# Kernel optimization log

Hardware: AMD Instinct MI355X
Metric: run time of the kernel (lower is better)

The kernel has to match this reference:

```python
import jax, jax.numpy as jnp
import numpy as np

B, N = 2, 1024
QDIM, HEADS, DHEAD, HID, CDIM = 512, 4, 64, 64, 16
INNER = HEADS * DHEAD
LN_EPS = 1e-5


def _gelu(t):
    return jax.nn.gelu(t, approximate=False)


def setup_inputs() -> dict:
    key = jax.random.key(0)
    ks = jax.random.split(key, 32)
    inp = {
        'x': jax.random.normal(ks[0], (B, N, QDIM), jnp.float32),
        'pair_mask': jax.random.randint(ks[1], (B, N, N), 0, 2) > 0,
        'valid_mask': jax.random.randint(ks[2], (B, N), 0, 2) > 0,
        'continuous_features': jax.random.normal(ks[3], (B, N, N, CDIM), jnp.float32),
        'distance_bucket': jax.random.randint(ks[4], (B, N, N), 0, 32),
        'direction_bucket': jax.random.randint(ks[5], (B, N, N), 0, 8),
        'role_pair_id': jax.random.randint(ks[6], (B, N, N), 0, 16),
        'hop_delta': jax.random.randint(ks[7], (B, N, N), 0, 16),
        'edge_type': jax.random.randint(ks[8], (B, N, N), 0, 8),
        'shortest_path_bucket': jax.random.randint(ks[9], (B, N, N), 0, 16),
        'same_cell_type': jax.random.randint(ks[10], (B, N, N), 0, 3),
        'degree_ids': jax.random.randint(ks[11], (B, N), 0, 66),
        'cell_type_ids': jax.random.randint(ks[12], (B, N), 0, 21),
    }
    s = 0.02
    # attention projections (stored as [in, out]; y = x @ W)
    inp['Wq'] = jax.random.normal(ks[13], (QDIM, INNER), jnp.float32) * s
    inp['Wk'] = jax.random.normal(ks[14], (QDIM, INNER), jnp.float32) * s
    inp['Wv'] = jax.random.normal(ks[15], (QDIM, INNER), jnp.float32) * s
    inp['Wo'] = jax.random.normal(ks[16], (INNER, QDIM), jnp.float32) * s
    inp['bo'] = jnp.zeros((QDIM,), jnp.float32)
    # continuous MLP
    inp['mlp_w1'] = jax.random.normal(ks[17], (CDIM, HID), jnp.float32) * s
    inp['mlp_b1'] = jnp.zeros((HID,), jnp.float32)
    inp['mlp_w2'] = jax.random.normal(ks[18], (HID, HID), jnp.float32) * s
    inp['mlp_b2'] = jnp.zeros((HID,), jnp.float32)
    # embedding tables
    inp['dist_emb'] = jax.random.normal(ks[19], (32, HID), jnp.float32) * s
    inp['dir_emb'] = jax.random.normal(ks[20], (8, HID), jnp.float32) * s
    inp['role_emb'] = jax.random.normal(ks[21], (16, HID), jnp.float32) * s
    inp['hop_emb'] = jax.random.normal(ks[22], (16, HID), jnp.float32) * s
    inp['edge_emb'] = jax.random.normal(ks[23], (8, HID), jnp.float32) * s
    inp['sp_emb'] = jax.random.normal(ks[24], (16, HID), jnp.float32) * s
    deg = jax.random.normal(ks[25], (66, HID), jnp.float32) * s
    inp['deg_emb'] = deg.at[0].set(0.0)  # padding_idx=0
    ct = jax.random.normal(ks[26], (21, HID), jnp.float32) * s
    inp['ct_emb'] = ct.at[0].set(0.0)    # padding_idx=0
    inp['same_emb'] = jax.random.normal(ks[27], (3, HID), jnp.float32) * s
    # output head: LayerNorm + Linear(HID -> HEADS)
    inp['ln_g'] = jnp.ones((HID,), jnp.float32)
    inp['ln_b'] = jnp.zeros((HID,), jnp.float32)
    inp['out_w'] = jax.random.normal(ks[28], (HID, HEADS), jnp.float32) * s
    inp['out_b'] = jnp.zeros((HEADS,), jnp.float32)
    return inp


def reference(x, pair_mask, valid_mask, continuous_features, distance_bucket,
              direction_bucket, role_pair_id, hop_delta, edge_type,
              shortest_path_bucket, same_cell_type, degree_ids, cell_type_ids,
              Wq, Wk, Wv, Wo, bo, mlp_w1, mlp_b1, mlp_w2, mlp_b2,
              dist_emb, dir_emb, role_emb, hop_emb, edge_emb, sp_emb,
              deg_emb, ct_emb, same_emb, ln_g, ln_b, out_w, out_b):
    b, n, _ = x.shape
    # --- PairwiseStructuralBias ---
    pair = _gelu(continuous_features @ mlp_w1 + mlp_b1) @ mlp_w2 + mlp_b2  # [b,n,n,HID]
    pair = pair + dist_emb[distance_bucket] + dir_emb[direction_bucket] \
               + role_emb[role_pair_id] + hop_emb[hop_delta] \
               + edge_emb[edge_type] + sp_emb[shortest_path_bucket] \
               + same_emb[same_cell_type]
    deg = deg_emb[degree_ids]          # [b,n,HID]
    pair = pair + deg[:, :, None, :] + deg[:, None, :, :]
    ct = ct_emb[cell_type_ids]         # [b,n,HID]
    pair = pair + ct[:, :, None, :] + ct[:, None, :, :]
    mu = pair.mean(-1, keepdims=True)
    var = ((pair - mu) ** 2).mean(-1, keepdims=True)
    ln = (pair - mu) * jax.lax.rsqrt(var + LN_EPS) * ln_g + ln_b
    bias = _gelu(ln) @ out_w + out_b                        # [b,n,n,H]
    bias = bias * pair_mask[..., None].astype(bias.dtype)
    bias = jnp.transpose(bias, (0, 3, 1, 2))                # [b,H,i,j]
    # --- attention ---
    def split_heads(t):
        return jnp.transpose(t.reshape(b, n, HEADS, DHEAD), (0, 2, 1, 3))
    q = split_heads(x @ Wq)
    k = split_heads(x @ Wk)
    v = split_heads(x @ Wv)
    scale = DHEAD ** -0.5
    logits = jnp.einsum('bhid,bhjd->bhij', q, k) * scale + bias
    eye = jnp.eye(n, dtype=bool)
    safe_pair_mask = pair_mask | ((~valid_mask)[:, :, None] & eye[None])
    neg = -jnp.finfo(logits.dtype).max
    logits = jnp.where(safe_pair_mask[:, None], logits, neg)
    attn = jax.nn.softmax(logits, axis=-1)
    attn = attn * pair_mask[:, None].astype(attn.dtype)
    attn = attn / jnp.clip(attn.sum(-1, keepdims=True), 1e-6)
    out = jnp.einsum('bhij,bhjd->bhid', attn, v)
    out = jnp.transpose(out, (0, 2, 1, 3)).reshape(b, n, INNER)
    out = out @ Wo + bo
    return out, attn, bias
```

## Files before the change

kernel.cpp:

```cpp
#include <hip/hip_runtime.h>
#include <float.h>
#include <math.h>


#define WS_PM    0u
#define WS_VM    2097152u
#define WS_W1TB  2100224u
#define WS_W2TB  2104320u
#define WS_OWBT  2112512u
#define WS_Q     4194304u
#define WS_KT    6291456u
#define WS_V     8388608u
#define WS_AO    10485760u

typedef __attribute__((ext_vector_type(8))) short short8;
typedef __attribute__((ext_vector_type(4))) float f32x4;

__device__ __forceinline__ unsigned short f2bf(float x) {
    unsigned u = __float_as_uint(x);
    u += 0x7fffu + ((u >> 16) & 1u);
    return (unsigned short)(u >> 16);
}
__device__ __forceinline__ unsigned cvt_pk_bf16(float lo, float hi) {
    unsigned r;
    asm("v_cvt_pk_bf16_f32 %0, %1, %2" : "=v"(r) : "v"(lo), "v"(hi));
    return r;
}
__device__ __forceinline__ float gelu_fast(float x) {
    float x2 = x * x;
    float u = x * fmaf(0.0713548135f, x2, 1.5957691216f);
    float e = __expf(-u);
    return x * __builtin_amdgcn_rcpf(1.0f + e);
}
__device__ __forceinline__ float4 fma4(float s, float4 a, float4 c) {
    c.x = fmaf(s, a.x, c.x); c.y = fmaf(s, a.y, c.y);
    c.z = fmaf(s, a.z, c.z); c.w = fmaf(s, a.w, c.w);
    return c;
}
__device__ __forceinline__ float wave_max(float v) {
#pragma unroll
    for (int m = 1; m < 64; m <<= 1) v = fmaxf(v, __shfl_xor(v, m));
    return v;
}
__device__ __forceinline__ float wave_sum(float v) {
#pragma unroll
    for (int m = 1; m < 64; m <<= 1) v += __shfl_xor(v, m);
    return v;
}
__device__ __forceinline__ float4 ldg4(const float* p, int boff) {
    return *(const float4*)((const char*)p + boff);
}
__device__ __forceinline__ float4 add4(float4 a, float4 b) {
    a.x += b.x; a.y += b.y; a.z += b.z; a.w += b.w;
    return a;
}

__global__ void prep_kernel(const float* __restrict__ w1, const float* __restrict__ w2,
                            const float* __restrict__ ow,
                            unsigned short* __restrict__ w1tb,
                            unsigned short* __restrict__ w2tb,
                            unsigned short* __restrict__ owbt) {
    int t = threadIdx.x;
    for (int i = t; i < 2048; i += 256) {
        int e = i >> 5, c = i & 31;
        float v = (c < 16) ? w1[c * 64 + e] : 0.f;
        w1tb[i] = f2bf(v);
    }
    for (int i = t; i < 4096; i += 256) {
        int d = i >> 6, e = i & 63;
        w2tb[i] = f2bf(w2[e * 64 + d]);
    }
    for (int i = t; i < 1024; i += 256) {
        int h = i >> 6, e = i & 63;
        owbt[i] = (h < 4) ? f2bf(ow[e * 4 + h]) : (unsigned short)0;
    }
}

__global__ __launch_bounds__(256) void mask_kernel(const void* __restrict__ pm_raw,
                                                   const void* __restrict__ vm_raw,
                                                   unsigned char* __restrict__ pm8,
                                                   unsigned char* __restrict__ vm8) {
    __shared__ int sflag;
    int t = threadIdx.x;
    if (t == 0) sflag = 0;
    __syncthreads();
    const unsigned* p32 = (const unsigned*)pm_raw;
    unsigned acc = 0;
    for (int k = t; k < 1024; k += 256) acc |= (p32[k] & ~1u);
    if (acc) sflag = 1;
    __syncthreads();
    bool u8 = (sflag != 0);
    size_t base = (size_t)blockIdx.x * 1024;
    const unsigned char* p8 = (const unsigned char*)pm_raw;
    const int* pi = (const int*)pm_raw;
    for (int k = t; k < 1024; k += 256) {
        size_t idx = base + (size_t)k;
        pm8[idx] = u8 ? (unsigned char)(p8[idx] != 0) : (unsigned char)(pi[idx] != 0);
    }
    if (blockIdx.x == 0) {
        const unsigned char* v8 = (const unsigned char*)vm_raw;
        const int* vi = (const int*)vm_raw;
        for (int k = t; k < 2048; k += 256)
            vm8[k] = u8 ? (unsigned char)(v8[k] != 0) : (unsigned char)(vi[k] != 0);
    }
}

__global__ __launch_bounds__(256) void qkv_kernel(const float* __restrict__ x,
        const float* __restrict__ Wq, const float* __restrict__ Wk, const float* __restrict__ Wv,
        float* __restrict__ q, float* __restrict__ kt, float* __restrict__ v) {
    __shared__ float As[32][68];
    __shared__ float Bs[32][68];
    int tid = threadIdx.x;
    int bx = blockIdx.x, by = blockIdx.y;
    int mat = bx >> 2;
    const float* __restrict__ W = (mat == 0) ? Wq : ((mat == 1) ? Wk : Wv);
    int col0 = (bx & 3) * 64;
    int row0 = by * 64;
    int tx = tid & 15, ty = tid >> 4;
    int lm = tid >> 3, lk = (tid & 7) * 4;
    int bn = (tid & 15) * 4, bk = tid >> 4;
    float4 acc0 = {0,0,0,0}, acc1 = acc0, acc2 = acc0, acc3 = acc0;
    for (int k0 = 0; k0 < 512; k0 += 32) {
        float4 a0 = *(const float4*)&x[(size_t)(row0 + lm) * 512 + k0 + lk];
        float4 a1 = *(const float4*)&x[(size_t)(row0 + lm + 32) * 512 + k0 + lk];
        float4 b0 = *(const float4*)&W[(size_t)(k0 + bk) * 256 + col0 + bn];
        float4 b1 = *(const float4*)&W[(size_t)(k0 + bk + 16) * 256 + col0 + bn];
        __syncthreads();
        As[lk + 0][lm] = a0.x; As[lk + 1][lm] = a0.y; As[lk + 2][lm] = a0.z; As[lk + 3][lm] = a0.w;
        As[lk + 0][lm + 32] = a1.x; As[lk + 1][lm + 32] = a1.y; As[lk + 2][lm + 32] = a1.z; As[lk + 3][lm + 32] = a1.w;
        *(float4*)&Bs[bk][bn] = b0;
        *(float4*)&Bs[bk + 16][bn] = b1;
        __syncthreads();
#pragma unroll
        for (int kk = 0; kk < 32; ++kk) {
            float4 av = *(const float4*)&As[kk][ty * 4];
            float4 bv = *(const float4*)&Bs[kk][tx * 4];
            acc0 = fma4(av.x, bv, acc0);
            acc1 = fma4(av.y, bv, acc1);
            acc2 = fma4(av.z, bv, acc2);
            acc3 = fma4(av.w, bv, acc3);
        }
    }
#pragma unroll
    for (int r = 0; r < 4; ++r) {
        float4 a = (r == 0) ? acc0 : ((r == 1) ? acc1 : ((r == 2) ? acc2 : acc3));
        int gr = row0 + ty * 4 + r;
        int b = gr >> 10, n = gr & 1023;
        float vals[4] = {a.x, a.y, a.z, a.w};
#pragma unroll
        for (int c = 0; c < 4; ++c) {
            int cc = col0 + tx * 4 + c;
            int h = cc >> 6, d = cc & 63;
            size_t bh = (size_t)(b * 4 + h);
            float val = vals[c];
            if (mat == 0)      q[(bh * 1024 + n) * 64 + d] = val;
            else if (mat == 1) kt[(bh * 64 + d) * 1024 + n] = val;
            else               v[(bh * 1024 + n) * 64 + d] = val;
        }
    }
}

__global__ __launch_bounds__(256, 4) void pair_kernel(
        const float* __restrict__ cf,
        const int* __restrict__ i_dist, const int* __restrict__ i_dir,
        const int* __restrict__ i_role, const int* __restrict__ i_hop,
        const int* __restrict__ i_edge, const int* __restrict__ i_sp,
        const int* __restrict__ i_same,
        const int* __restrict__ deg_ids, const int* __restrict__ ct_ids,
        const float* __restrict__ e_dist, const float* __restrict__ e_dir,
        const float* __restrict__ e_role, const float* __restrict__ e_hop,
        const float* __restrict__ e_edge, const float* __restrict__ e_sp,
        const float* __restrict__ e_same, const float* __restrict__ e_deg,
        const float* __restrict__ e_ct,
        const float* __restrict__ b1, const float* __restrict__ b2,
        const unsigned short* __restrict__ w1tb, const unsigned short* __restrict__ w2tb,
        const unsigned short* __restrict__ owbt,
        const float* __restrict__ lng, const float* __restrict__ lnb,
        const float* __restrict__ outb,
        const unsigned char* __restrict__ pm,
        float* __restrict__ bias_out) {
    __shared__ alignas(8) unsigned short es[64 * 68];
    __shared__ alignas(16) unsigned short h1b[64 * 64];
    __shared__ alignas(16) unsigned short cfb[64 * 32];
    __shared__ float prm[192];
    __shared__ float bias_lds[576];

    int tid = threadIdx.x;
    int wu = __builtin_amdgcn_readfirstlane(tid >> 6);
    int lane = tid & 63;
    int m = lane & 15, g = lane >> 4;
    size_t row0 = (size_t)blockIdx.x * 64;
    int b  = (int)(row0 >> 20);
    int i  = (int)((row0 >> 10) & 1023);
    int j0 = (int)(row0 & 1023);
    int r0 = (int)row0;

    for (int k = lane; k < 192; k += 64) {
        float v;
        if (k < 64) v = b1[k];
        else if (k < 128) v = lng[k - 64];
        else v = lnb[k - 128];
        prm[k] = v;
    }
    {
        int rl = wu * 16 + (lane >> 2);
        int ch = (lane & 3) * 4;
        float4 c4 = *(const float4*)&cf[((size_t)(r0 + rl)) * 16 + ch];
        ushort4 u;
        u.x = f2bf(c4.x); u.y = f2bf(c4.y); u.z = f2bf(c4.z); u.w = f2bf(c4.w);
        *(ushort4*)&cfb[rl * 32 + ch] = u;
        ushort4 z = {0, 0, 0, 0};
        *(ushort4*)&cfb[rl * 32 + 16 + ch] = z;
    }
    {
        int di = deg_ids[b * 1024 + i];
        int ci = ct_ids[b * 1024 + i];
        int c = lane & 15;
        int rsub = lane >> 4;
        int choff = c * 16;
        float4 base4 = add4(add4(ldg4(b2, choff), ldg4(e_deg + di * 64, choff)),
                            ldg4(e_ct + ci * 64, choff));
#pragma unroll
        for (int it = 0; it < 4; ++it) {
            int row = wu * 16 + it * 4 + rsub;
            int gr = r0 + row;
            int q0 = i_dist[gr], q1 = i_dir[gr], q2 = i_role[gr], q3 = i_hop[gr],
                q4 = i_edge[gr], q5 = i_sp[gr], q6 = i_same[gr];
            int q7 = deg_ids[b * 1024 + j0 + row];
            int q8 = ct_ids[b * 1024 + j0 + row];
            float4 a = base4;
            a = add4(a, ldg4(e_dist, q0 * 256 + choff));
            a = add4(a, ldg4(e_dir,  q1 * 256 + choff));
            a = add4(a, ldg4(e_role, q2 * 256 + choff));
            a = add4(a, ldg4(e_hop,  q3 * 256 + choff));
            a = add4(a, ldg4(e_edge, q4 * 256 + choff));
            a = add4(a, ldg4(e_sp,   q5 * 256 + choff));
            a = add4(a, ldg4(e_same, q6 * 256 + choff));
            a = add4(a, ldg4(e_deg,  q7 * 256 + choff));
            a = add4(a, ldg4(e_ct,   q8 * 256 + choff));
            uint2 pk;
            pk.x = cvt_pk_bf16(a.x, a.y);
            pk.y = cvt_pk_bf16(a.z, a.w);
            *(uint2*)((char*)es + row * 136 + c * 8) = pk;
        }
    }

    f32x4 acc1[4] = {{0,0,0,0},{0,0,0,0},{0,0,0,0},{0,0,0,0}};
    {
        short8 afrag = *(const short8*)&cfb[(wu * 16 + m) * 32 + g * 8];
#pragma unroll
        for (int t = 0; t < 4; ++t) {
            short8 bfrag = *(const short8*)&w1tb[(t * 16 + m) * 32 + g * 8];
            acc1[t] = __builtin_amdgcn_mfma_f32_16x16x32_bf16(afrag, bfrag, acc1[t], 0, 0, 0);
        }
    }
#pragma unroll
    for (int tp = 0; tp < 2; ++tp) {
#pragma unroll
        for (int r = 0; r < 4; ++r) {
            int rowl = wu * 16 + g * 4 + r;
            int c0 = tp * 32 + m, c1 = c0 + 16;
            float g0 = gelu_fast(acc1[tp * 2][r] + prm[c0]);
            float g1 = gelu_fast(acc1[tp * 2 + 1][r] + prm[c1]);
            unsigned pk = cvt_pk_bf16(g0, g1);
            int swz = (rowl & 7) << 4;
            *(unsigned short*)((char*)h1b + ((rowl * 128 + c0 * 2) ^ swz)) = (unsigned short)pk;
            *(unsigned short*)((char*)h1b + ((rowl * 128 + c1 * 2) ^ swz)) = (unsigned short)(pk >> 16);
        }
    }

    f32x4 acc2[4] = {{0,0,0,0},{0,0,0,0},{0,0,0,0},{0,0,0,0}};
#pragma unroll
    for (int ks = 0; ks < 2; ++ks) {
        int rowl = wu * 16 + m;
        int byte = (rowl * 128 + ks * 64 + g * 16) ^ ((m & 7) << 4);
        short8 afrag = *(const short8*)((const char*)h1b + byte);
#pragma unroll
        for (int t = 0; t < 4; ++t) {
            short8 bfrag = *(const short8*)&w2tb[(t * 16 + m) * 64 + ks * 32 + g * 8];
            acc2[t] = __builtin_amdgcn_mfma_f32_16x16x32_bf16(afrag, bfrag, acc2[t], 0, 0, 0);
        }
    }

    float pv[4][4];
    float s[4] = {0,0,0,0}, s2[4] = {0,0,0,0};
#pragma unroll
    for (int t = 0; t < 4; ++t) {
#pragma unroll
        for (int r = 0; r < 4; ++r) {
            int rowl = wu * 16 + g * 4 + r;
            float esv = __uint_as_float((unsigned)es[rowl * 68 + t * 16 + m] << 16);
            float v = acc2[t][r] + esv;
            pv[t][r] = v;
            s[r] += v; s2[r] = fmaf(v, v, s2[r]);
        }
    }
#pragma unroll
    for (int o = 1; o < 16; o <<= 1) {
#pragma unroll
        for (int r = 0; r < 4; ++r) {
            s[r]  += __shfl_xor(s[r], o);
            s2[r] += __shfl_xor(s2[r], o);
        }
    }
    float mu[4], rs[4];
#pragma unroll
    for (int r = 0; r < 4; ++r) {
        mu[r] = s[r] * 0.015625f;
        float var = fmaxf(s2[r] * 0.015625f - mu[r] * mu[r], 0.f);
        rs[r] = rsqrtf(var + 1e-5f);
    }
#pragma unroll
    for (int tp = 0; tp < 2; ++tp) {
#pragma unroll
        for (int r = 0; r < 4; ++r) {
            int rowl = wu * 16 + g * 4 + r;
            int c0 = tp * 32 + m, c1 = c0 + 16;
            float l0 = fmaf((pv[tp * 2][r] - mu[r]) * rs[r], prm[64 + c0], prm[128 + c0]);
            float l1 = fmaf((pv[tp * 2 + 1][r] - mu[r]) * rs[r], prm[64 + c1], prm[128 + c1]);
            unsigned pk = cvt_pk_bf16(gelu_fast(l0), gelu_fast(l1));
            int swz = (rowl & 7) << 4;
            *(unsigned short*)((char*)h1b + ((rowl * 128 + c0 * 2) ^ swz)) = (unsigned short)pk;
            *(unsigned short*)((char*)h1b + ((rowl * 128 + c1 * 2) ^ swz)) = (unsigned short)(pk >> 16);
        }
    }
    f32x4 accH = {0,0,0,0};
#pragma unroll
    for (int ks = 0; ks < 2; ++ks) {
        int rowl = wu * 16 + m;
        int byte = (rowl * 128 + ks * 64 + g * 16) ^ ((m & 7) << 4);
        short8 afrag = *(const short8*)((const char*)h1b + byte);
        short8 bfrag = *(const short8*)&owbt[m * 64 + ks * 32 + g * 8];
        accH = __builtin_amdgcn_mfma_f32_16x16x32_bf16(afrag, bfrag, accH, 0, 0, 0);
    }
    if (m < 4) {
        float ob = outb[m];
#pragma unroll
        for (int r = 0; r < 4; ++r) {
            int rowl = wu * 16 + g * 4 + r;
            bias_lds[rowl * 9 + m] = accH[r] + ob;
        }
    }
    __syncthreads();
    {
        float pmv = pm[r0 + lane] ? 1.f : 0.f;
        size_t ob = (size_t)(b * 4 + wu) * 1048576u + (size_t)i * 1024u + (size_t)(j0 + lane);
        bias_out[ob] = bias_lds[lane * 9 + wu] * pmv;
    }
}

__global__ __launch_bounds__(256) void attn_kernel(
        const float* __restrict__ q, const float* __restrict__ kt, const float* __restrict__ v,
        const unsigned char* __restrict__ pm, const unsigned char* __restrict__ vm,
        const float* __restrict__ bias, float* __restrict__ attn, float* __restrict__ ao) {
    __shared__ float pbuf[4][1024];
    int tid = threadIdx.x;
    int w = tid >> 6, lane = tid & 63;
    int blk = blockIdx.x;
    int it = blk & 63;
    int bh = blk >> 6;
    int b = bh >> 2, h = bh & 3;
    int i0 = __builtin_amdgcn_readfirstlane(it * 16 + w * 4);
    const float* __restrict__ qr = q + ((size_t)bh * 1024 + i0) * 64;
    const float4* __restrict__ kt4 = (const float4*)kt;
    const float4* __restrict__ v4 = (const float4*)v;
    const float4* __restrict__ bias4 = (const float4*)bias;
    float4* __restrict__ attn4 = (float4*)attn;
    float4* __restrict__ ao4 = (float4*)ao;

    float4 lg[4][4];
#pragma unroll
    for (int jt = 0; jt < 4; ++jt) {
        float4 a0 = {0,0,0,0}, a1 = a0, a2 = a0, a3 = a0;
#pragma unroll 4
        for (int d = 0; d < 64; ++d) {
            float4 kv = kt4[((size_t)bh * 64 + d) * 256 + jt * 64 + lane];
            a0 = fma4(qr[d], kv, a0);
            a1 = fma4(qr[64 + d], kv, a1);
            a2 = fma4(qr[128 + d], kv, a2);
            a3 = fma4(qr[192 + d], kv, a3);
        }
#pragma unroll
        for (int rr = 0; rr < 4; ++rr) {
            float4 acc = (rr == 0) ? a0 : ((rr == 1) ? a1 : ((rr == 2) ? a2 : a3));
            float4 bv = bias4[((size_t)bh * 1024 + i0 + rr) * 256 + jt * 64 + lane];
            float4 l;
            l.x = fmaf(acc.x, 0.125f, bv.x);
            l.y = fmaf(acc.y, 0.125f, bv.y);
            l.z = fmaf(acc.z, 0.125f, bv.z);
            l.w = fmaf(acc.w, 0.125f, bv.w);
            lg[rr][jt] = l;
        }
    }
#pragma unroll
    for (int rr = 0; rr < 4; ++rr) {
        int i = i0 + rr;
        bool vld = vm[b * 1024 + i] != 0;
        float4 ev[4];
        float pmax = -FLT_MAX;
#pragma unroll
        for (int jt = 0; jt < 4; ++jt) {
            uchar4 m4 = *(const uchar4*)&pm[((size_t)b * 1024 + i) * 1024 + jt * 256 + lane * 4];
            int jb = jt * 256 + lane * 4;
            float4 l = lg[rr][jt];
            l.x = (m4.x || (!vld && (jb + 0) == i)) ? l.x : -FLT_MAX;
            l.y = (m4.y || (!vld && (jb + 1) == i)) ? l.y : -FLT_MAX;
            l.z = (m4.z || (!vld && (jb + 2) == i)) ? l.z : -FLT_MAX;
            l.w = (m4.w || (!vld && (jb + 3) == i)) ? l.w : -FLT_MAX;
            lg[rr][jt] = l;
            pmax = fmaxf(pmax, fmaxf(fmaxf(l.x, l.y), fmaxf(l.z, l.w)));
        }
        pmax = wave_max(pmax);
        float s1sum = 0.f;
#pragma unroll
        for (int jt = 0; jt < 4; ++jt) {
            float4 l = lg[rr][jt];
            float4 e;
            e.x = __expf(l.x - pmax); e.y = __expf(l.y - pmax);
            e.z = __expf(l.z - pmax); e.w = __expf(l.w - pmax);
            ev[jt] = e;
            s1sum += (e.x + e.y) + (e.z + e.w);
        }
        s1sum = wave_sum(s1sum);
        float inv1 = 1.f / s1sum;
        float s2sum = 0.f;
#pragma unroll
        for (int jt = 0; jt < 4; ++jt) {
            uchar4 m4 = *(const uchar4*)&pm[((size_t)b * 1024 + i) * 1024 + jt * 256 + lane * 4];
            float4 e = ev[jt];
            e.x = m4.x ? e.x * inv1 : 0.f;
            e.y = m4.y ? e.y * inv1 : 0.f;
            e.z = m4.z ? e.z * inv1 : 0.f;
            e.w = m4.w ? e.w * inv1 : 0.f;
            ev[jt] = e;
            s2sum += (e.x + e.y) + (e.z + e.w);
        }
        s2sum = wave_sum(s2sum);
        float inv2 = 1.f / fmaxf(s2sum, 1e-6f);
#pragma unroll
        for (int jt = 0; jt < 4; ++jt) {
            float4 e = ev[jt];
            e.x *= inv2; e.y *= inv2; e.z *= inv2; e.w *= inv2;
            attn4[((size_t)bh * 1024 + i) * 256 + jt * 64 + lane] = e;
            *(float4*)&pbuf[w][jt * 256 + lane * 4] = e;
        }
        __syncthreads();
        int dq = lane & 15, grp = lane >> 4;
        float4 o = {0,0,0,0};
#pragma unroll 4
        for (int t = 0; t < 64; ++t) {
            int jj = grp * 4 + t * 16;
            float4 p4 = *(const float4*)&pbuf[w][jj];
            float4 v0 = v4[((size_t)bh * 1024 + jj + 0) * 16 + dq];
            float4 v1 = v4[((size_t)bh * 1024 + jj + 1) * 16 + dq];
            float4 v2 = v4[((size_t)bh * 1024 + jj + 2) * 16 + dq];
            float4 v3 = v4[((size_t)bh * 1024 + jj + 3) * 16 + dq];
            o = fma4(p4.x, v0, o); o = fma4(p4.y, v1, o);
            o = fma4(p4.z, v2, o); o = fma4(p4.w, v3, o);
        }
        o.x += __shfl_xor(o.x, 16); o.y += __shfl_xor(o.y, 16);
        o.z += __shfl_xor(o.z, 16); o.w += __shfl_xor(o.w, 16);
        o.x += __shfl_xor(o.x, 32); o.y += __shfl_xor(o.y, 32);
        o.z += __shfl_xor(o.z, 32); o.w += __shfl_xor(o.w, 32);
        if (grp == 0) ao4[((size_t)(b * 1024 + i) * 4 + h) * 16 + dq] = o;
        __syncthreads();
    }
}

__global__ __launch_bounds__(256) void outproj_kernel(
        const float* __restrict__ ao, const float* __restrict__ Wo,
        const float* __restrict__ bo, float* __restrict__ out) {
    __shared__ float As[32][68];
    __shared__ float Bs[32][68];
    int tid = threadIdx.x;
    int bx = blockIdx.x, by = blockIdx.y;
    int col0 = bx * 64, row0 = by * 64;
    int tx = tid & 15, ty = tid >> 4;
    int lm = tid >> 3, lk = (tid & 7) * 4;
    int bn = (tid & 15) * 4, bk = tid >> 4;
    float4 acc0 = {0,0,0,0}, acc1 = acc0, acc2 = acc0, acc3 = acc0;
    for (int k0 = 0; k0 < 256; k0 += 32) {
        float4 a0 = *(const float4*)&ao[(size_t)(row0 + lm) * 256 + k0 + lk];
        float4 a1 = *(const float4*)&ao[(size_t)(row0 + lm + 32) * 256 + k0 + lk];
        float4 b0 = *(const float4*)&Wo[(size_t)(k0 + bk) * 512 + col0 + bn];
        float4 b1 = *(const float4*)&Wo[(size_t)(k0 + bk + 16) * 512 + col0 + bn];
        __syncthreads();
        As[lk + 0][lm] = a0.x; As[lk + 1][lm] = a0.y; As[lk + 2][lm] = a0.z; As[lk + 3][lm] = a0.w;
        As[lk + 0][lm + 32] = a1.x; As[lk + 1][lm + 32] = a1.y; As[lk + 2][lm + 32] = a1.z; As[lk + 3][lm + 32] = a1.w;
        *(float4*)&Bs[bk][bn] = b0;
        *(float4*)&Bs[bk + 16][bn] = b1;
        __syncthreads();
#pragma unroll
        for (int kk = 0; kk < 32; ++kk) {
            float4 av = *(const float4*)&As[kk][ty * 4];
            float4 bv = *(const float4*)&Bs[kk][tx * 4];
            acc0 = fma4(av.x, bv, acc0);
            acc1 = fma4(av.y, bv, acc1);
            acc2 = fma4(av.z, bv, acc2);
            acc3 = fma4(av.w, bv, acc3);
        }
    }
#pragma unroll
    for (int r = 0; r < 4; ++r) {
        float4 a = (r == 0) ? acc0 : ((r == 1) ? acc1 : ((r == 2) ? acc2 : acc3));
        int gr = row0 + ty * 4 + r;
        float vals[4] = {a.x, a.y, a.z, a.w};
#pragma unroll
        for (int c = 0; c < 4; ++c) {
            int gc = col0 + tx * 4 + c;
            out[(size_t)gr * 512 + gc] = vals[c] + bo[gc];
        }
    }
}

extern "C" void kernel_launch(void* const* d_in, const int* in_sizes, int n_in,
                              void* d_out, int out_size, void* d_ws, size_t ws_size,
                              hipStream_t stream) {
    (void)in_sizes; (void)n_in; (void)out_size; (void)ws_size;
    const float* x    = (const float*)d_in[0];
    const void*  pmr  = d_in[1];
    const void*  vmr  = d_in[2];
    const float* cf   = (const float*)d_in[3];
    const int* dist_b = (const int*)d_in[4];
    const int* dir_b  = (const int*)d_in[5];
    const int* role_b = (const int*)d_in[6];
    const int* hop_b  = (const int*)d_in[7];
    const int* edge_b = (const int*)d_in[8];
    const int* sp_b   = (const int*)d_in[9];
    const int* same_b = (const int*)d_in[10];
    const int* deg_ids = (const int*)d_in[11];
    const int* ct_ids  = (const int*)d_in[12];
    const float* Wq = (const float*)d_in[13];
    const float* Wk = (const float*)d_in[14];
    const float* Wv = (const float*)d_in[15];
    const float* Wo = (const float*)d_in[16];
    const float* bo = (const float*)d_in[17];
    const float* w1 = (const float*)d_in[18];
    const float* b1 = (const float*)d_in[19];
    const float* w2 = (const float*)d_in[20];
    const float* b2 = (const float*)d_in[21];
    const float* e_dist = (const float*)d_in[22];
    const float* e_dir  = (const float*)d_in[23];
    const float* e_role = (const float*)d_in[24];
    const float* e_hop  = (const float*)d_in[25];
    const float* e_edge = (const float*)d_in[26];
    const float* e_sp   = (const float*)d_in[27];
    const float* e_deg  = (const float*)d_in[28];
    const float* e_ct   = (const float*)d_in[29];
    const float* e_same = (const float*)d_in[30];
    const float* lng  = (const float*)d_in[31];
    const float* lnb  = (const float*)d_in[32];
    const float* ow   = (const float*)d_in[33];
    const float* outb = (const float*)d_in[34];

    char* ws = (char*)d_ws;
    unsigned char* pm8 = (unsigned char*)(ws + WS_PM);
    unsigned char* vm8 = (unsigned char*)(ws + WS_VM);
    unsigned short* w1tb = (unsigned short*)(ws + WS_W1TB);
    unsigned short* w2tb = (unsigned short*)(ws + WS_W2TB);
    unsigned short* owbt = (unsigned short*)(ws + WS_OWBT);
    float* q   = (float*)(ws + WS_Q);
    float* kt  = (float*)(ws + WS_KT);
    float* v   = (float*)(ws + WS_V);
    float* ao  = (float*)(ws + WS_AO);

    float* out  = (float*)d_out;
    float* attn = out + 1048576;
    float* bias = out + 9437184;

    hipLaunchKernelGGL(prep_kernel, dim3(1), dim3(256), 0, stream, w1, w2, ow, w1tb, w2tb, owbt);
    hipLaunchKernelGGL(mask_kernel, dim3(2048), dim3(256), 0, stream, pmr, vmr, pm8, vm8);
    hipLaunchKernelGGL(qkv_kernel, dim3(12, 32), dim3(256), 0, stream, x, Wq, Wk, Wv, q, kt, v);
    hipLaunchKernelGGL(pair_kernel, dim3(32768), dim3(256), 0, stream,
                       cf, dist_b, dir_b, role_b, hop_b, edge_b, sp_b, same_b, deg_ids, ct_ids,
                       e_dist, e_dir, e_role, e_hop, e_edge, e_sp, e_same, e_deg, e_ct,
                       b1, b2, w1tb, w2tb, owbt, lng, lnb, outb, pm8, bias);
    hipLaunchKernelGGL(attn_kernel, dim3(512), dim3(256), 0, stream,
                       q, kt, v, pm8, vm8, bias, attn, ao);
    hipLaunchKernelGGL(outproj_kernel, dim3(8, 32), dim3(256), 0, stream, ao, Wo, bo, out);
}
```

Before: 535.9 us.

## Transpose pair-kernel MFMAs to keep rows per lane and drop LDS staging

Swaps the MFMA operand order for the second MLP and output projections so each lane holds a full row's channels. LayerNorm statistics then need only two cross-lane shuffles, and the bias can be written straight to global memory. The continuous-feature A fragment is built in registers instead of going through LDS, and the bias staging buffer and block barrier are removed. The edge-embedding buffer gets an XOR swizzle, and launch bounds rise to 8 waves per SIMD for occupancy, which may cause register spills.

```diff
diff --git a/kernel.cpp b/kernel.cpp
--- a/kernel.cpp
+++ b/kernel.cpp
@@ -160,7 +160,7 @@
     }
 }
 
-__global__ __launch_bounds__(256, 4) void pair_kernel(
+__global__ __launch_bounds__(256, 8) void pair_kernel(
         const float* __restrict__ cf,
         const int* __restrict__ i_dist, const int* __restrict__ i_dir,
         const int* __restrict__ i_role, const int* __restrict__ i_hop,
@@ -179,11 +179,9 @@
         const float* __restrict__ outb,
         const unsigned char* __restrict__ pm,
         float* __restrict__ bias_out) {
-    __shared__ alignas(8) unsigned short es[64 * 68];
+    __shared__ alignas(16) unsigned short es[64 * 64];
     __shared__ alignas(16) unsigned short h1b[64 * 64];
-    __shared__ alignas(16) unsigned short cfb[64 * 32];
-    __shared__ float prm[192];
-    __shared__ float bias_lds[576];
+    __shared__ alignas(16) float prm[192];
 
     int tid = threadIdx.x;
     int wu = __builtin_amdgcn_readfirstlane(tid >> 6);
@@ -194,6 +192,7 @@
     int i  = (int)((row0 >> 10) & 1023);
     int j0 = (int)(row0 & 1023);
     int r0 = (int)row0;
+    int rowl = wu * 16 + m;
 
     for (int k = lane; k < 192; k += 64) {
         float v;
@@ -202,27 +201,31 @@
         else v = lnb[k - 128];
         prm[k] = v;
     }
+
+    short8 afrag1;
     {
-        int rl = wu * 16 + (lane >> 2);
-        int ch = (lane & 3) * 4;
-        float4 c4 = *(const float4*)&cf[((size_t)(r0 + rl)) * 16 + ch];
-        ushort4 u;
-        u.x = f2bf(c4.x); u.y = f2bf(c4.y); u.z = f2bf(c4.z); u.w = f2bf(c4.w);
-        *(ushort4*)&cfb[rl * 32 + ch] = u;
-        ushort4 z = {0, 0, 0, 0};
-        *(ushort4*)&cfb[rl * 32 + 16 + ch] = z;
-    }
+        if (g < 2) {
+            const float4* cp = (const float4*)&cf[((size_t)(r0 + rowl)) * 16 + g * 8];
+            float4 c0 = cp[0], c1 = cp[1];
+            unsigned p0 = cvt_pk_bf16(c0.x, c0.y), p1 = cvt_pk_bf16(c0.z, c0.w);
+            unsigned p2 = cvt_pk_bf16(c1.x, c1.y), p3 = cvt_pk_bf16(c1.z, c1.w);
+            int4 tmp = { (int)p0, (int)p1, (int)p2, (int)p3 };
+            afrag1 = *(short8*)&tmp;
+        } else {
+            short8 z = {0,0,0,0,0,0,0,0};
+            afrag1 = z;
+        }
+    }
+
     {
         int di = deg_ids[b * 1024 + i];
         int ci = ct_ids[b * 1024 + i];
-        int c = lane & 15;
-        int rsub = lane >> 4;
-        int choff = c * 16;
+        int choff = m * 16;
         float4 base4 = add4(add4(ldg4(b2, choff), ldg4(e_deg + di * 64, choff)),
                             ldg4(e_ct + ci * 64, choff));
 #pragma unroll
         for (int it = 0; it < 4; ++it) {
-            int row = wu * 16 + it * 4 + rsub;
+            int row = wu * 16 + it * 4 + g;
             int gr = r0 + row;
             int q0 = i_dist[gr], q1 = i_dir[gr], q2 = i_role[gr], q3 = i_hop[gr],
                 q4 = i_edge[gr], q5 = i_sp[gr], q6 = i_same[gr];
@@ -241,111 +244,96 @@
             uint2 pk;
             pk.x = cvt_pk_bf16(a.x, a.y);
             pk.y = cvt_pk_bf16(a.z, a.w);
-            *(uint2*)((char*)es + row * 136 + c * 8) = pk;
+            *(uint2*)((char*)es + ((row * 128 + m * 8) ^ ((row & 7) << 4))) = pk;
         }
     }
 
     f32x4 acc1[4] = {{0,0,0,0},{0,0,0,0},{0,0,0,0},{0,0,0,0}};
-    {
-        short8 afrag = *(const short8*)&cfb[(wu * 16 + m) * 32 + g * 8];
-#pragma unroll
-        for (int t = 0; t < 4; ++t) {
-            short8 bfrag = *(const short8*)&w1tb[(t * 16 + m) * 32 + g * 8];
-            acc1[t] = __builtin_amdgcn_mfma_f32_16x16x32_bf16(afrag, bfrag, acc1[t], 0, 0, 0);
-        }
+#pragma unroll
+    for (int t = 0; t < 4; ++t) {
+        short8 bfrag = *(const short8*)&w1tb[(t * 16 + m) * 32 + g * 8];
+        acc1[t] = __builtin_amdgcn_mfma_f32_16x16x32_bf16(afrag1, bfrag, acc1[t], 0, 0, 0);
     }
 #pragma unroll
     for (int tp = 0; tp < 2; ++tp) {
 #pragma unroll
         for (int r = 0; r < 4; ++r) {
-            int rowl = wu * 16 + g * 4 + r;
+            int rw = wu * 16 + g * 4 + r;
             int c0 = tp * 32 + m, c1 = c0 + 16;
             float g0 = gelu_fast(acc1[tp * 2][r] + prm[c0]);
             float g1 = gelu_fast(acc1[tp * 2 + 1][r] + prm[c1]);
             unsigned pk = cvt_pk_bf16(g0, g1);
-            int swz = (rowl & 7) << 4;
-            *(unsigned short*)((char*)h1b + ((rowl * 128 + c0 * 2) ^ swz)) = (unsigned short)pk;
-            *(unsigned short*)((char*)h1b + ((rowl * 128 + c1 * 2) ^ swz)) = (unsigned short)(pk >> 16);
+            int swz = (rw & 7) << 4;
+            *(unsigned short*)((char*)h1b + ((rw * 128 + c0 * 2) ^ swz)) = (unsigned short)pk;
+            *(unsigned short*)((char*)h1b + ((rw * 128 + c1 * 2) ^ swz)) = (unsigned short)(pk >> 16);
         }
     }
 
     f32x4 acc2[4] = {{0,0,0,0},{0,0,0,0},{0,0,0,0},{0,0,0,0}};
 #pragma unroll
     for (int ks = 0; ks < 2; ++ks) {
-        int rowl = wu * 16 + m;
         int byte = (rowl * 128 + ks * 64 + g * 16) ^ ((m & 7) << 4);
-        short8 afrag = *(const short8*)((const char*)h1b + byte);
+        short8 hfrag = *(const short8*)((const char*)h1b + byte);
 #pragma unroll
         for (int t = 0; t < 4; ++t) {
-            short8 bfrag = *(const short8*)&w2tb[(t * 16 + m) * 64 + ks * 32 + g * 8];
-            acc2[t] = __builtin_amdgcn_mfma_f32_16x16x32_bf16(afrag, bfrag, acc2[t], 0, 0, 0);
+            short8 wfrag = *(const short8*)&w2tb[(t * 16 + m) * 64 + ks * 32 + g * 8];
+            acc2[t] = __builtin_amdgcn_mfma_f32_16x16x32_bf16(wfrag, hfrag, acc2[t], 0, 0, 0);
         }
     }
 
     float pv[4][4];
-    float s[4] = {0,0,0,0}, s2[4] = {0,0,0,0};
+    float s = 0.f, s2 = 0.f;
 #pragma unroll
     for (int t = 0; t < 4; ++t) {
-#pragma unroll
-        for (int r = 0; r < 4; ++r) {
-            int rowl = wu * 16 + g * 4 + r;
-            float esv = __uint_as_float((unsigned)es[rowl * 68 + t * 16 + m] << 16);
-            float v = acc2[t][r] + esv;
-            pv[t][r] = v;
-            s[r] += v; s2[r] = fmaf(v, v, s2[r]);
-        }
-    }
-#pragma unroll
-    for (int o = 1; o < 16; o <<= 1) {
-#pragma unroll
-        for (int r = 0; r < 4; ++r) {
-            s[r]  += __shfl_xor(s[r], o);
-            s2[r] += __shfl_xor(s2[r], o);
-        }
-    }
-    float mu[4], rs[4];
-#pragma unroll
-    for (int r = 0; r < 4; ++r) {
-        mu[r] = s[r] * 0.015625f;
-        float var = fmaxf(s2[r] * 0.015625f - mu[r] * mu[r], 0.f);
-        rs[r] = rsqrtf(var + 1e-5f);
-    }
-#pragma unroll
-    for (int tp = 0; tp < 2; ++tp) {
-#pragma unroll
-        for (int r = 0; r < 4; ++r) {
-            int rowl = wu * 16 + g * 4 + r;
-            int c0 = tp * 32 + m, c1 = c0 + 16;
-            float l0 = fmaf((pv[tp * 2][r] - mu[r]) * rs[r], prm[64 + c0], prm[128 + c0]);
-            float l1 = fmaf((pv[tp * 2 + 1][r] - mu[r]) * rs[r], prm[64 + c1], prm[128 + c1]);
-            unsigned pk = cvt_pk_bf16(gelu_fast(l0), gelu_fast(l1));
-            int swz = (rowl & 7) << 4;
-            *(unsigned short*)((char*)h1b + ((rowl * 128 + c0 * 2) ^ swz)) = (unsigned short)pk;
-            *(unsigned short*)((char*)h1b + ((rowl * 128 + c1 * 2) ^ swz)) = (unsigned short)(pk >> 16);
-        }
-    }
+        uint2 u = *(const uint2*)((const char*)es +
+                   ((rowl * 128 + t * 32 + g * 8) ^ ((rowl & 7) << 4)));
+        float e0 = __uint_as_float(u.x << 16);
+        float e1 = __uint_as_float(u.x & 0xffff0000u);
+        float e2 = __uint_as_float(u.y << 16);
+        float e3 = __uint_as_float(u.y & 0xffff0000u);
+        pv[t][0] = acc2[t][0] + e0;
+        pv[t][1] = acc2[t][1] + e1;
+        pv[t][2] = acc2[t][2] + e2;
+        pv[t][3] = acc2[t][3] + e3;
+#pragma unroll
+        for (int r = 0; r < 4; ++r) { s += pv[t][r]; s2 = fmaf(pv[t][r], pv[t][r], s2); }
+    }
+    s  += __shfl_xor(s, 16);  s2 += __shfl_xor(s2, 16);
+    s  += __shfl_xor(s, 32);  s2 += __shfl_xor(s2, 32);
+    float mu = s * 0.015625f;
+    float var = fmaxf(s2 * 0.015625f - mu * mu, 0.f);
+    float rs = rsqrtf(var + 1e-5f);
+
+#pragma unroll
+    for (int t = 0; t < 4; ++t) {
+        float4 lg4 = *(const float4*)&prm[64 + t * 16 + 4 * g];
+        float4 lb4 = *(const float4*)&prm[128 + t * 16 + 4 * g];
+        float g0 = gelu_fast(fmaf((pv[t][0] - mu) * rs, lg4.x, lb4.x));
+        float g1 = gelu_fast(fmaf((pv[t][1] - mu) * rs, lg4.y, lb4.y));
+        float g2 = gelu_fast(fmaf((pv[t][2] - mu) * rs, lg4.z, lb4.z));
+        float g3 = gelu_fast(fmaf((pv[t][3] - mu) * rs, lg4.w, lb4.w));
+        uint2 pk;
+        pk.x = cvt_pk_bf16(g0, g1);
+        pk.y = cvt_pk_bf16(g2, g3);
+        *(uint2*)((char*)h1b + ((rowl * 128 + t * 32 + g * 8) ^ ((m & 7) << 4))) = pk;
+    }
+
     f32x4 accH = {0,0,0,0};
 #pragma unroll
     for (int ks = 0; ks < 2; ++ks) {
-        int rowl = wu * 16 + m;
         int byte = (rowl * 128 + ks * 64 + g * 16) ^ ((m & 7) << 4);
-        short8 afrag = *(const short8*)((const char*)h1b + byte);
-        short8 bfrag = *(const short8*)&owbt[m * 64 + ks * 32 + g * 8];
-        accH = __builtin_amdgcn_mfma_f32_16x16x32_bf16(afrag, bfrag, accH, 0, 0, 0);
-    }
-    if (m < 4) {
-        float ob = outb[m];
-#pragma unroll
-        for (int r = 0; r < 4; ++r) {
-            int rowl = wu * 16 + g * 4 + r;
-            bias_lds[rowl * 9 + m] = accH[r] + ob;
-        }
-    }
-    __syncthreads();
-    {
-        float pmv = pm[r0 + lane] ? 1.f : 0.f;
-        size_t ob = (size_t)(b * 4 + wu) * 1048576u + (size_t)i * 1024u + (size_t)(j0 + lane);
-        bias_out[ob] = bias_lds[lane * 9 + wu] * pmv;
+        short8 gfrag = *(const short8*)((const char*)h1b + byte);
+        short8 ofrag = *(const short8*)&owbt[m * 64 + ks * 32 + g * 8];
+        accH = __builtin_amdgcn_mfma_f32_16x16x32_bf16(ofrag, gfrag, accH, 0, 0, 0);
+    }
+    if (g == 0) {
+        float pmv = pm[r0 + rowl] ? 1.f : 0.f;
+        size_t ob = (size_t)b * 4194304u + (size_t)i * 1024u + (size_t)(j0 + rowl);
+        float ob0 = outb[0], ob1 = outb[1], ob2 = outb[2], ob3 = outb[3];
+        bias_out[ob]             = (accH[0] + ob0) * pmv;
+        bias_out[ob + 1048576u]  = (accH[1] + ob1) * pmv;
+        bias_out[ob + 2097152u]  = (accH[2] + ob2) * pmv;
+        bias_out[ob + 3145728u]  = (accH[3] + ob3) * pmv;
     }
 }
 
```

New measurement: 606.9 us. 1.13x slower.

## Replace embedding gathers with one-hot MFMA against concatenated bf16 table

Applied to the files above, without the earlier changes.

The nine per-pair embedding lookups are no longer done as scattered float4 gathers and adds. Each pair row now builds a multi-hot bf16 vector in LDS and multiplies it by a concatenated transposed table (prepared once in prep_kernel) with MFMA, accumulating straight into the second-layer accumulator initialised with b2 plus the per-i embeddings. The continuous-feature A fragment is also loaded directly into registers instead of going through LDS. This trades many irregular global loads for more MFMA work, more LDS use (about 25KB for the one-hot buffers) and bf16 rounding of the table values, and it relies on the invalid-index-free inputs.

```diff
diff --git a/kernel.cpp b/kernel.cpp
--- a/kernel.cpp
+++ b/kernel.cpp
@@ -8,6 +8,7 @@
 #define WS_W1TB  2100224u
 #define WS_W2TB  2104320u
 #define WS_OWBT  2112512u
+#define WS_TT    2116608u
 #define WS_Q     4194304u
 #define WS_KT    6291456u
 #define WS_V     8388608u
@@ -47,19 +48,18 @@
     for (int m = 1; m < 64; m <<= 1) v += __shfl_xor(v, m);
     return v;
 }
-__device__ __forceinline__ float4 ldg4(const float* p, int boff) {
-    return *(const float4*)((const char*)p + boff);
-}
-__device__ __forceinline__ float4 add4(float4 a, float4 b) {
-    a.x += b.x; a.y += b.y; a.z += b.z; a.w += b.w;
-    return a;
-}
 
 __global__ void prep_kernel(const float* __restrict__ w1, const float* __restrict__ w2,
                             const float* __restrict__ ow,
+                            const float* __restrict__ e_dist, const float* __restrict__ e_dir,
+                            const float* __restrict__ e_role, const float* __restrict__ e_hop,
+                            const float* __restrict__ e_edge, const float* __restrict__ e_sp,
+                            const float* __restrict__ e_same, const float* __restrict__ e_deg,
+                            const float* __restrict__ e_ct,
                             unsigned short* __restrict__ w1tb,
                             unsigned short* __restrict__ w2tb,
-                            unsigned short* __restrict__ owbt) {
+                            unsigned short* __restrict__ owbt,
+                            unsigned short* __restrict__ ttcat) {
     int t = threadIdx.x;
     for (int i = t; i < 2048; i += 256) {
         int e = i >> 5, c = i & 31;
@@ -73,6 +73,20 @@
     for (int i = t; i < 1024; i += 256) {
         int h = i >> 6, e = i & 63;
         owbt[i] = (h < 4) ? f2bf(ow[e * 4 + h]) : (unsigned short)0;
+    }
+    for (int i = t; i < 64 * 192; i += 256) {
+        int c = i / 192, e = i - (i / 192) * 192;
+        float v = 0.f;
+        if (e < 32)       v = e_dist[e * 64 + c];
+        else if (e < 40)  v = e_dir[(e - 32) * 64 + c];
+        else if (e < 56)  v = e_role[(e - 40) * 64 + c];
+        else if (e < 72)  v = e_hop[(e - 56) * 64 + c];
+        else if (e < 80)  v = e_edge[(e - 72) * 64 + c];
+        else if (e < 96)  v = e_sp[(e - 80) * 64 + c];
+        else if (e < 99)  v = e_same[(e - 96) * 64 + c];
+        else if (e < 165) v = e_deg[(e - 99) * 64 + c];
+        else if (e < 186) v = e_ct[(e - 165) * 64 + c];
+        ttcat[i] = f2bf(v);
     }
 }
 
@@ -167,23 +181,21 @@
         const int* __restrict__ i_edge, const int* __restrict__ i_sp,
         const int* __restrict__ i_same,
         const int* __restrict__ deg_ids, const int* __restrict__ ct_ids,
-        const float* __restrict__ e_dist, const float* __restrict__ e_dir,
-        const float* __restrict__ e_role, const float* __restrict__ e_hop,
-        const float* __restrict__ e_edge, const float* __restrict__ e_sp,
-        const float* __restrict__ e_same, const float* __restrict__ e_deg,
-        const float* __restrict__ e_ct,
-        const float* __restrict__ b1, const float* __restrict__ b2,
+        const float* __restrict__ e_deg, const float* __restrict__ e_ct,
+        const float* __restrict__ b2,
         const unsigned short* __restrict__ w1tb, const unsigned short* __restrict__ w2tb,
-        const unsigned short* __restrict__ owbt,
+        const unsigned short* __restrict__ owbt, const unsigned short* __restrict__ ttcat,
+        const float* __restrict__ b1,
         const float* __restrict__ lng, const float* __restrict__ lnb,
         const float* __restrict__ outb,
         const unsigned char* __restrict__ pm,
         float* __restrict__ bias_out) {
-    __shared__ alignas(8) unsigned short es[64 * 68];
+    __shared__ alignas(16) char aoh[4 * 6400];
     __shared__ alignas(16) unsigned short h1b[64 * 64];
-    __shared__ alignas(16) unsigned short cfb[64 * 32];
     __shared__ float prm[192];
     __shared__ float bias_lds[576];
+    __shared__ unsigned long long sptr[9];
+    __shared__ int soff[9];
 
     int tid = threadIdx.x;
     int wu = __builtin_amdgcn_readfirstlane(tid >> 6);
@@ -194,6 +206,7 @@
     int i  = (int)((row0 >> 10) & 1023);
     int j0 = (int)(row0 & 1023);
     int r0 = (int)row0;
+    char* aw = aoh + wu * 6400;
 
     for (int k = lane; k < 192; k += 64) {
         float v;
@@ -202,74 +215,100 @@
         else v = lnb[k - 128];
         prm[k] = v;
     }
+    if (lane < 9) {
+        const void* p; int of;
+        switch (lane) {
+            case 0: p = i_dist; of = 0;   break;
+            case 1: p = i_dir;  of = 32;  break;
+            case 2: p = i_role; of = 40;  break;
+            case 3: p = i_hop;  of = 56;  break;
+            case 4: p = i_edge; of = 72;  break;
+            case 5: p = i_sp;   of = 80;  break;
+            case 6: p = i_same; of = 96;  break;
+            case 7: p = deg_ids; of = 99; break;
+            default: p = ct_ids; of = 165; break;
+        }
+        long basei = (lane < 7) ? (long)r0 : (long)(b * 1024 + j0);
+        sptr[lane] = (unsigned long long)((const char*)p + basei * 4);
+        soff[lane] = of;
+    }
+
+    short8 afrag1;
     {
-        int rl = wu * 16 + (lane >> 2);
-        int ch = (lane & 3) * 4;
-        float4 c4 = *(const float4*)&cf[((size_t)(r0 + rl)) * 16 + ch];
-        ushort4 u;
-        u.x = f2bf(c4.x); u.y = f2bf(c4.y); u.z = f2bf(c4.z); u.w = f2bf(c4.w);
-        *(ushort4*)&cfb[rl * 32 + ch] = u;
-        ushort4 z = {0, 0, 0, 0};
-        *(ushort4*)&cfb[rl * 32 + 16 + ch] = z;
-    }
+        if (g < 2) {
+            const float4* cp = (const float4*)&cf[((size_t)(r0 + wu * 16 + m)) * 16 + g * 8];
+            float4 c0 = cp[0], c1 = cp[1];
+            unsigned p0 = cvt_pk_bf16(c0.x, c0.y), p1 = cvt_pk_bf16(c0.z, c0.w);
+            unsigned p2 = cvt_pk_bf16(c1.x, c1.y), p3 = cvt_pk_bf16(c1.z, c1.w);
+            int4 tmp = { (int)p0, (int)p1, (int)p2, (int)p3 };
+            afrag1 = *(short8*)&tmp;
+        } else {
+            short8 z = {0,0,0,0,0,0,0,0};
+            afrag1 = z;
+        }
+    }
+
+    f32x4 acc2[4];
     {
         int di = deg_ids[b * 1024 + i];
         int ci = ct_ids[b * 1024 + i];
-        int c = lane & 15;
-        int rsub = lane >> 4;
-        int choff = c * 16;
-        float4 base4 = add4(add4(ldg4(b2, choff), ldg4(e_deg + di * 64, choff)),
-                            ldg4(e_ct + ci * 64, choff));
-#pragma unroll
-        for (int it = 0; it < 4; ++it) {
-            int row = wu * 16 + it * 4 + rsub;
-            int gr = r0 + row;
-            int q0 = i_dist[gr], q1 = i_dir[gr], q2 = i_role[gr], q3 = i_hop[gr],
-                q4 = i_edge[gr], q5 = i_sp[gr], q6 = i_same[gr];
-            int q7 = deg_ids[b * 1024 + j0 + row];
-            int q8 = ct_ids[b * 1024 + j0 + row];
-            float4 a = base4;
-            a = add4(a, ldg4(e_dist, q0 * 256 + choff));
-            a = add4(a, ldg4(e_dir,  q1 * 256 + choff));
-            a = add4(a, ldg4(e_role, q2 * 256 + choff));
-            a = add4(a, ldg4(e_hop,  q3 * 256 + choff));
-            a = add4(a, ldg4(e_edge, q4 * 256 + choff));
-            a = add4(a, ldg4(e_sp,   q5 * 256 + choff));
-            a = add4(a, ldg4(e_same, q6 * 256 + choff));
-            a = add4(a, ldg4(e_deg,  q7 * 256 + choff));
-            a = add4(a, ldg4(e_ct,   q8 * 256 + choff));
-            uint2 pk;
-            pk.x = cvt_pk_bf16(a.x, a.y);
-            pk.y = cvt_pk_bf16(a.z, a.w);
-            *(uint2*)((char*)es + row * 136 + c * 8) = pk;
+#pragma unroll
+        for (int t = 0; t < 4; ++t) {
+            int c = t * 16 + m;
+            float bv = b2[c] + e_deg[di * 64 + c] + e_ct[ci * 64 + c];
+            f32x4 ini = {bv, bv, bv, bv};
+            acc2[t] = ini;
+        }
+    }
+
+    {
+        uint4 z = {0u, 0u, 0u, 0u};
+#pragma unroll
+        for (int rr = 0; rr < 6; ++rr) *(uint4*)(aw + rr * 1024 + lane * 16) = z;
+        if (lane < 16) *(uint4*)(aw + 6144 + lane * 16) = z;
+    }
+#pragma unroll
+    for (int ps = 0; ps < 3; ++ps) {
+        int t = ps * 4 + g;
+        if (t < 9) {
+            unsigned long long p = sptr[t];
+            int of = soff[t];
+            int idx = *(const int*)((const char*)p + (size_t)(wu * 16 + m) * 4);
+            *(unsigned short*)(aw + m * 400 + (of + idx) * 2) = (unsigned short)0x3F80;
         }
     }
 
     f32x4 acc1[4] = {{0,0,0,0},{0,0,0,0},{0,0,0,0},{0,0,0,0}};
-    {
-        short8 afrag = *(const short8*)&cfb[(wu * 16 + m) * 32 + g * 8];
-#pragma unroll
-        for (int t = 0; t < 4; ++t) {
-            short8 bfrag = *(const short8*)&w1tb[(t * 16 + m) * 32 + g * 8];
-            acc1[t] = __builtin_amdgcn_mfma_f32_16x16x32_bf16(afrag, bfrag, acc1[t], 0, 0, 0);
-        }
+#pragma unroll
+    for (int t = 0; t < 4; ++t) {
+        short8 bfrag = *(const short8*)&w1tb[(t * 16 + m) * 32 + g * 8];
+        acc1[t] = __builtin_amdgcn_mfma_f32_16x16x32_bf16(afrag1, bfrag, acc1[t], 0, 0, 0);
     }
 #pragma unroll
     for (int tp = 0; tp < 2; ++tp) {
 #pragma unroll
         for (int r = 0; r < 4; ++r) {
-            int rowl = wu * 16 + g * 4 + r;
+            int rw = wu * 16 + g * 4 + r;
             int c0 = tp * 32 + m, c1 = c0 + 16;
             float g0 = gelu_fast(acc1[tp * 2][r] + prm[c0]);
             float g1 = gelu_fast(acc1[tp * 2 + 1][r] + prm[c1]);
             unsigned pk = cvt_pk_bf16(g0, g1);
-            int swz = (rowl & 7) << 4;
-            *(unsigned short*)((char*)h1b + ((rowl * 128 + c0 * 2) ^ swz)) = (unsigned short)pk;
-            *(unsigned short*)((char*)h1b + ((rowl * 128 + c1 * 2) ^ swz)) = (unsigned short)(pk >> 16);
-        }
-    }
-
-    f32x4 acc2[4] = {{0,0,0,0},{0,0,0,0},{0,0,0,0},{0,0,0,0}};
+            int swz = (rw & 7) << 4;
+            *(unsigned short*)((char*)h1b + ((rw * 128 + c0 * 2) ^ swz)) = (unsigned short)pk;
+            *(unsigned short*)((char*)h1b + ((rw * 128 + c1 * 2) ^ swz)) = (unsigned short)(pk >> 16);
+        }
+    }
+
+#pragma unroll
+    for (int ks = 0; ks < 6; ++ks) {
+        short8 ae = *(const short8*)(aw + m * 400 + ks * 64 + g * 16);
+#pragma unroll
+        for (int t = 0; t < 4; ++t) {
+            short8 be = *(const short8*)&ttcat[(size_t)(t * 16 + m) * 192 + ks * 32 + g * 8];
+            acc2[t] = __builtin_amdgcn_mfma_f32_16x16x32_bf16(ae, be, acc2[t], 0, 0, 0);
+        }
+    }
+
 #pragma unroll
     for (int ks = 0; ks < 2; ++ks) {
         int rowl = wu * 16 + m;
@@ -282,16 +321,12 @@
         }
     }
 
-    float pv[4][4];
     float s[4] = {0,0,0,0}, s2[4] = {0,0,0,0};
 #pragma unroll
     for (int t = 0; t < 4; ++t) {
 #pragma unroll
         for (int r = 0; r < 4; ++r) {
-            int rowl = wu * 16 + g * 4 + r;
-            float esv = __uint_as_float((unsigned)es[rowl * 68 + t * 16 + m] << 16);
-            float v = acc2[t][r] + esv;
-            pv[t][r] = v;
+            float v = acc2[t][r];
             s[r] += v; s2[r] = fmaf(v, v, s2[r]);
         }
     }
@@ -316,8 +351,8 @@
         for (int r = 0; r < 4; ++r) {
             int rowl = wu * 16 + g * 4 + r;
             int c0 = tp * 32 + m, c1 = c0 + 16;
-            float l0 = fmaf((pv[tp * 2][r] - mu[r]) * rs[r], prm[64 + c0], prm[128 + c0]);
-            float l1 = fmaf((pv[tp * 2 + 1][r] - mu[r]) * rs[r], prm[64 + c1], prm[128 + c1]);
+            float l0 = fmaf((acc2[tp * 2][r] - mu[r]) * rs[r], prm[64 + c0], prm[128 + c0]);
+            float l1 = fmaf((acc2[tp * 2 + 1][r] - mu[r]) * rs[r], prm[64 + c1], prm[128 + c1]);
             unsigned pk = cvt_pk_bf16(gelu_fast(l0), gelu_fast(l1));
             int swz = (rowl & 7) << 4;
             *(unsigned short*)((char*)h1b + ((rowl * 128 + c0 * 2) ^ swz)) = (unsigned short)pk;
@@ -559,6 +594,7 @@
     unsigned short* w1tb = (unsigned short*)(ws + WS_W1TB);
     unsigned short* w2tb = (unsigned short*)(ws + WS_W2TB);
     unsigned short* owbt = (unsigned short*)(ws + WS_OWBT);
+    unsigned short* ttcat = (unsigned short*)(ws + WS_TT);
     float* q   = (float*)(ws + WS_Q);
     float* kt  = (float*)(ws + WS_KT);
     float* v   = (float*)(ws + WS_V);
@@ -568,13 +604,15 @@
     float* attn = out + 1048576;
     float* bias = out + 9437184;
 
-    hipLaunchKernelGGL(prep_kernel, dim3(1), dim3(256), 0, stream, w1, w2, ow, w1tb, w2tb, owbt);
+    hipLaunchKernelGGL(prep_kernel, dim3(1), dim3(256), 0, stream, w1, w2, ow,
+                       e_dist, e_dir, e_role, e_hop, e_edge, e_sp, e_same, e_deg, e_ct,
+                       w1tb, w2tb, owbt, ttcat);
     hipLaunchKernelGGL(mask_kernel, dim3(2048), dim3(256), 0, stream, pmr, vmr, pm8, vm8);
     hipLaunchKernelGGL(qkv_kernel, dim3(12, 32), dim3(256), 0, stream, x, Wq, Wk, Wv, q, kt, v);
     hipLaunchKernelGGL(pair_kernel, dim3(32768), dim3(256), 0, stream,
                        cf, dist_b, dir_b, role_b, hop_b, edge_b, sp_b, same_b, deg_ids, ct_ids,
-                       e_dist, e_dir, e_role, e_hop, e_edge, e_sp, e_same, e_deg, e_ct,
-                       b1, b2, w1tb, w2tb, owbt, lng, lnb, outb, pm8, bias);
+                       e_deg, e_ct, b2, w1tb, w2tb, owbt, ttcat,
+                       b1, lng, lnb, outb, pm8, bias);
     hipLaunchKernelGGL(attn_kernel, dim3(512), dim3(256), 0, stream,
                        q, kt, v, pm8, vm8, bias, attn, ao);
     hipLaunchKernelGGL(outproj_kernel, dim3(8, 32), dim3(256), 0, stream, ao, Wo, bo, out);
```

Measured after the change: 752.0 us. 40.3% more time.
